# Kernel tuning notes

Hardware: AMD Instinct MI355X
Metric: run time of the kernel (lower is better)

Reference implementation:

```python
import jax, jax.numpy as jnp
import numpy as np

EMBEDDING_DIM = 256
NUM_EMBEDDINGS = 8192
COMMITMENT_COST = 0.25
DECAY = 0.99
EPSILON = 1e-5


def setup_inputs() -> dict:
    key = jax.random.key(0)
    k1, k2 = jax.random.split(key)
    inputs = jax.random.normal(k1, (16, 32, 32, EMBEDDING_DIM), dtype=jnp.float32)
    # VarianceScaling(distribution='uniform'), fan_in scaling over [D, K]
    limit = float(np.sqrt(3.0 / EMBEDDING_DIM))
    embeddings = jax.random.uniform(k2, (EMBEDDING_DIM, NUM_EMBEDDINGS),
                                    minval=-limit, maxval=limit, dtype=jnp.float32)
    return {
        'inputs': inputs,
        'embeddings': embeddings,
        'ema_cs_hidden': jnp.zeros((NUM_EMBEDDINGS,), jnp.float32),
        'ema_dw_hidden': embeddings,  # hk initializes ema_dw to the embeddings
        'counter': 0,
        'is_training': 1,
    }


def reference(inputs, embeddings, ema_cs_hidden, ema_dw_hidden, counter, is_training):
    flat = inputs.reshape(-1, EMBEDDING_DIM)                        # [N, D]
    distances = (jnp.sum(flat ** 2, axis=1, keepdims=True)
                 - 2.0 * (flat @ embeddings)
                 + jnp.sum(embeddings ** 2, axis=0, keepdims=True))  # [N, K]
    encoding_indices = jnp.argmax(-distances, axis=1)                # [N]
    encodings = jax.nn.one_hot(encoding_indices, NUM_EMBEDDINGS,
                               dtype=distances.dtype)                # [N, K]
    idx = encoding_indices.reshape(inputs.shape[:-1])
    quantized = embeddings.T[idx]                                    # gather codebook
    e_latent_loss = jnp.mean((jax.lax.stop_gradient(quantized) - inputs) ** 2)
    loss = COMMITMENT_COST * e_latent_loss

    if is_training:
        # haiku ExponentialMovingAverage with zero-debias
        new_counter = counter + 1
        debias = 1.0 - DECAY ** new_counter
        cs_hidden = ema_cs_hidden * DECAY + jnp.sum(encodings, axis=0) * (1.0 - DECAY)
        cs_avg = cs_hidden / debias                                  # [K]
        dw = flat.T @ encodings                                      # [D, K] scatter-add as GEMM
        dw_hidden = ema_dw_hidden * DECAY + dw * (1.0 - DECAY)
        dw_avg = dw_hidden / debias
        n = jnp.sum(cs_avg)
        cs_norm = (cs_avg + EPSILON) / (n + NUM_EMBEDDINGS * EPSILON) * n
        new_embeddings = dw_avg / cs_norm[None, :]                   # [D, K]
    else:
        new_embeddings = embeddings

    # straight-through estimator
    quantized_st = inputs + jax.lax.stop_gradient(quantized - inputs)
    avg_probs = jnp.mean(encodings, axis=0)
    perplexity = jnp.exp(-jnp.sum(avg_probs * jnp.log(avg_probs + 1e-10)))
    return (quantized_st, loss, perplexity, idx, new_embeddings)
```

## Files before the change

### kernel.cpp

```cpp
#include <hip/hip_runtime.h>
#include <math.h>

#define DD 256
#define KK 8192
#define NN 16384
#define DECAYF 0.99f
#define EPSF 1e-5f
#define TAU 4e-3f

#define O_Q    0
#define O_LOSS 4194304
#define O_PERP 4194305
#define O_IDX  4194306
#define O_EMB  4210690

typedef float f32x4 __attribute__((ext_vector_type(4)));
typedef _Float16 f16x8 __attribute__((ext_vector_type(8)));

__device__ __forceinline__ unsigned short f2h(float f) {
  union { _Float16 h; unsigned short u; } c;
  c.h = (_Float16)f;
  return c.u;
}

__device__ __forceinline__ void gll16(const void* g, void* l) {
  __builtin_amdgcn_global_load_lds((const __attribute__((address_space(1))) void*)g,
                                   (__attribute__((address_space(3))) void*)l, 16, 0, 0);
}

#define DPPI(x, ctrl) __builtin_amdgcn_update_dpp((x), (x), (ctrl), 0xf, 0xf, true)
#define DPPF(x, ctrl) __int_as_float(__builtin_amdgcn_update_dpp(__float_as_int(x), __float_as_int(x), (ctrl), 0xf, 0xf, true))

__global__ void k_convert_xe(const float* __restrict__ x, unsigned short* __restrict__ Ah,
                             const float* __restrict__ emb, unsigned short* __restrict__ Eh,
                             float* __restrict__ embT, float* __restrict__ esqp,
                             unsigned long long* __restrict__ keysR,
                             float* __restrict__ counts, float* __restrict__ loss_part,
                             int* __restrict__ listc) {
  __shared__ float ld[32 * 33];
  int bx = blockIdx.x;
  int t = threadIdx.x;
  if (bx < 4096) {
    int i = bx * 256 + t;
    float4 v = ((const float4*)x)[i];
    ushort4 h;
    h.x = f2h(v.x); h.y = f2h(v.y); h.z = f2h(v.z); h.w = f2h(v.w);
    ((ushort4*)Ah)[i] = h;
    if (bx < 64) {
      keysR[bx * 256 + t] = ~0ull;
    } else if (bx < 96) {
      counts[(bx - 64) * 256 + t] = 0.f;
    } else if (bx == 96) {
      loss_part[t] = 0.f;
      if (t == 0) *listc = 0;
    }
    return;
  }
  int eb = bx - 4096;
  int k0 = (eb & 255) * 32, d0b = eb >> 8;
  {
    int din = t >> 3, kq = (t & 7) * 4;
    float4 v = *(const float4*)(emb + (size_t)(d0b * 32 + din) * KK + k0 + kq);
    ld[din * 33 + kq + 0] = v.x; ld[din * 33 + kq + 1] = v.y;
    ld[din * 33 + kq + 2] = v.z; ld[din * 33 + kq + 3] = v.w;
  }
  __syncthreads();
  int kout = t >> 3, dq = (t & 7) * 4;
  float f0 = ld[(dq + 0) * 33 + kout], f1 = ld[(dq + 1) * 33 + kout];
  float f2 = ld[(dq + 2) * 33 + kout], f3 = ld[(dq + 3) * 33 + kout];
  size_t o = (size_t)(k0 + kout) * DD + d0b * 32 + dq;
  float4 fv; fv.x = f0; fv.y = f1; fv.z = f2; fv.w = f3;
  *(float4*)(embT + o) = fv;
  ushort4 hv;
  hv.x = f2h(f0); hv.y = f2h(f1); hv.z = f2h(f2); hv.w = f2h(f3);
  *(ushort4*)(Eh + o) = hv;
  float p = (f0 * f0 + f1 * f1) + (f2 * f2 + f3 * f3);
  p += __shfl_xor(p, 1, 64);
  p += __shfl_xor(p, 2, 64);
  p += __shfl_xor(p, 4, 64);
  if ((t & 7) == 0) esqp[(size_t)(k0 + kout) * 8 + d0b] = p;
}

__launch_bounds__(256, 2)
__global__ void k_dist_mfma(const unsigned short* __restrict__ Ah, const unsigned short* __restrict__ Bh,
                            const float* __restrict__ esqp,
                            float* __restrict__ part1, float* __restrict__ part2,
                            int* __restrict__ partidx) {
  __shared__ __align__(16) unsigned short sB[8192];
  __shared__ float sEq[128];

  const int tid = threadIdx.x;
  const int w = tid >> 6, lane = tid & 63;
  const int kb = blockIdx.x, nb = blockIdx.y;
  const int row0 = nb * 128, col0 = kb * 128;
  const int m = lane & 15, q = lane >> 4;

  {
    int col = tid >> 1, half = tid & 1;
    const float4* ep = (const float4*)esqp + (size_t)(col0 + col) * 2 + half;
    float4 s = *ep;
    float p = (s.x + s.y) + (s.z + s.w);
    p += __shfl_xor(p, 1, 64);
    if (half == 0) sEq[col] = p;
  }

  size_t gB[4];
  int lbB[4];
  #pragma unroll
  for (int s = 0; s < 4; ++s) {
    int g = w * 4 + s;
    int r = g * 8 + (lane >> 3);
    int c = (lane & 7) ^ (r & 7);
    gB[s] = (size_t)(col0 + r) * DD + c * 8;
    lbB[s] = g * 512;
  }

  const unsigned short* pA0 = Ah + (size_t)(row0 + w * 32 + m) * DD + q * 8;
  const unsigned short* pA1 = pA0 + 16 * DD;

  f32x4 acc[2][8];
  #pragma unroll
  for (int i = 0; i < 2; ++i)
    #pragma unroll
    for (int j = 0; j < 8; ++j) acc[i][j] = (f32x4)0.f;

  for (int it = 0; it < 4; ++it) {
    const int d0 = it * 64;
    __syncthreads();
    #pragma unroll
    for (int s = 0; s < 4; ++s) gll16(Bh + gB[s] + d0, sB + lbB[s]);
    f16x8 a[2][2];
    #pragma unroll
    for (int kk = 0; kk < 2; ++kk) {
      a[kk][0] = *(const f16x8*)(pA0 + d0 + kk * 32);
      a[kk][1] = *(const f16x8*)(pA1 + d0 + kk * 32);
    }
    __syncthreads();
    #pragma unroll
    for (int kk = 0; kk < 2; ++kk) {
      #pragma unroll
      for (int j = 0; j < 8; ++j) {
        int cn = j * 16 + m;
        int slot = (kk * 4 + q) ^ (cn & 7);
        f16x8 b = *(const f16x8*)(sB + cn * 64 + slot * 8);
        acc[0][j] = __builtin_amdgcn_mfma_f32_16x16x32_f16(a[kk][0], b, acc[0][j], 0, 0, 0);
        acc[1][j] = __builtin_amdgcn_mfma_f32_16x16x32_f16(a[kk][1], b, acc[1][j], 0, 0, 0);
      }
    }
  }

  float eq[8];
  #pragma unroll
  for (int j = 0; j < 8; ++j) eq[j] = sEq[j * 16 + m];

  #define RSTAGE(CTRL) {                                  \
    float ov = DPPF(m1, CTRL);                            \
    int   oi = DPPI(bi, CTRL);                            \
    float o2 = DPPF(m2, CTRL);                            \
    m2 = fminf(fminf(m2, o2), fmaxf(m1, ov));             \
    bool p = ov < m1;                                     \
    m1 = fminf(m1, ov);                                   \
    bi = p ? oi : bi;                                     \
  }
  #pragma unroll
  for (int i = 0; i < 2; ++i) {
    #pragma unroll
    for (int reg = 0; reg < 4; ++reg) {
      float m1 = 3.402823466e+38f, m2 = 3.402823466e+38f;
      int bi = 0;
      #pragma unroll
      for (int j = 0; j < 8; ++j) {
        float dd = fmaf(-2.0f, acc[i][j][reg], eq[j]);
        bool p = dd < m1;
        m2 = fminf(m2, fmaxf(dd, m1));
        m1 = fminf(m1, dd);
        bi = p ? (col0 + j * 16 + m) : bi;
      }
      RSTAGE(0xB1)
      RSTAGE(0x4E)
      RSTAGE(0x141)
      RSTAGE(0x140)
      if (m == 0) {
        int prow = row0 + w * 32 + i * 16 + q * 4 + reg;
        int pidx = prow * 64 + kb;
        part1[pidx] = m1; part2[pidx] = m2; partidx[pidx] = bi;
      }
    }
  }
  #undef RSTAGE
}

__global__ void k_argmin2(float* __restrict__ part1, float* __restrict__ part2,
                          const int* __restrict__ partidx, int* __restrict__ idxw,
                          int* __restrict__ listc, int* __restrict__ list) {
  int w = threadIdx.x >> 6, l = threadIdx.x & 63;
  int row = blockIdx.x * 4 + w;
  int f = blockIdx.x * 256 + threadIdx.x;
  float m1 = part1[f], m2 = part2[f];
  int bi = partidx[f];
  part1[f] = 0.f;
  part2[f] = 0.f;
  #pragma unroll
  for (int st = 1; st < 64; st <<= 1) {
    float ov = __shfl_xor(m1, st, 64);
    int   oi = __shfl_xor(bi, st, 64);
    float o2 = __shfl_xor(m2, st, 64);
    m2 = fminf(fminf(m2, o2), fmaxf(m1, ov));
    bool p = ov < m1;
    m1 = fminf(m1, ov);
    bi = p ? oi : bi;
  }
  if (l == 0) {
    idxw[row] = bi;
    if (m2 - m1 < TAU) { int pos = atomicAdd(listc, 1); list[pos] = row; }
  }
}

__global__ void k_rescore(const float* __restrict__ x, const float* __restrict__ emb,
                          const int* __restrict__ listc, const int* __restrict__ list,
                          unsigned long long* __restrict__ keysR) {
  __shared__ float se[8192];
  __shared__ double red[256];
  const int t = threadIdx.x;
  const int k0 = blockIdx.x * 32;
  int cnt = *listc;
  if ((int)blockIdx.y >= cnt) return;
  #pragma unroll
  for (int i = 0; i < 32; ++i) {
    int elem = i * 256 + t;
    int d = elem >> 5, c = elem & 31;
    se[d * 32 + c] = emb[(size_t)d * KK + k0 + c];
  }
  __syncthreads();
  const int c = t & 31, p = t >> 5;
  for (int li = blockIdx.y; li < cnt; li += gridDim.y) {
    int row = list[li];
    const float* xr = x + (size_t)row * DD;
    double acc = 0.0;
    #pragma unroll
    for (int j = 0; j < 32; ++j) {
      int d = p * 32 + j;
      double df = (double)xr[d] - (double)se[d * 32 + c];
      acc = fma(df, df, acc);
    }
    red[c * 8 + p] = acc;
    __syncthreads();
    if (t < 64) {
      unsigned long long key = ~0ull;
      if (t < 32) {
        double dist = 0.0;
        #pragma unroll
        for (int qq = 0; qq < 8; ++qq) dist += red[t * 8 + qq];
        key = ((unsigned long long)__double_as_longlong(dist) & ~0x1FFFull)
              | (unsigned long long)(k0 + t);
      }
      #pragma unroll
      for (int s = 1; s < 64; s <<= 1) {
        unsigned long long o = __shfl_xor(key, s, 64);
        if (o < key) key = o;
      }
      if (t == 0) atomicMin(&keysR[row], key);
    }
    __syncthreads();
  }
}

__global__ void k_gather(const float* __restrict__ x, const float* __restrict__ embT,
                         const int* __restrict__ idxw, const unsigned long long* __restrict__ keysR,
                         const int* __restrict__ train,
                         float* __restrict__ outq, float* __restrict__ outidx,
                         float* __restrict__ dwT, float* __restrict__ counts,
                         float* __restrict__ loss_part) {
  int w = threadIdx.x >> 6, l = threadIdx.x & 63;
  int n = blockIdx.x * 4 + w;
  unsigned long long kv = keysR[n];
  int k = (kv != ~0ull) ? (int)(kv & 0x1FFFull) : idxw[n];
  float4 xv = ((const float4*)(x + (size_t)n * DD))[l];
  float4 qv = ((const float4*)(embT + (size_t)k * DD))[l];
  int d = l * 4;

  ((float4*)(outq + (size_t)n * DD))[l] = qv;

  float e0 = qv.x - xv.x, e1 = qv.y - xv.y, e2 = qv.z - xv.z, e3 = qv.w - xv.w;
  float ls = (e0 * e0 + e1 * e1) + (e2 * e2 + e3 * e3);

  if (*train) {
    const float wdw = 1.0f - DECAYF;
    float* base = dwT + (size_t)k * DD + d;
    atomicAdd(base + 0, xv.x * wdw);
    atomicAdd(base + 1, xv.y * wdw);
    atomicAdd(base + 2, xv.z * wdw);
    atomicAdd(base + 3, xv.w * wdw);
  }

  #pragma unroll
  for (int s = 1; s < 64; s <<= 1) ls += __shfl_xor(ls, s, 64);
  if (l == 0) {
    atomicAdd(&loss_part[blockIdx.x & 255], ls);
    atomicAdd(&counts[k], 1.0f);
    outidx[n] = (float)k;
  }
}

__global__ void k_final(const float* __restrict__ dwT, const float* __restrict__ ema_dw,
                        const float* __restrict__ emb, const float* __restrict__ counts,
                        const float* __restrict__ ema_cs, const float* __restrict__ loss_part,
                        const int* __restrict__ counter, const int* __restrict__ train,
                        float* __restrict__ out4, float* __restrict__ outloss,
                        float* __restrict__ outperp) {
  __shared__ float ld[32 * 33];
  __shared__ float s_red[4], s_l[4], s_e[4];
  __shared__ float csn_s[32];
  int t = threadIdx.x;
  int k0 = blockIdx.x * 32, d0 = blockIdx.y * 32;
  int w = t >> 6, lane = t & 63;

  if (blockIdx.x == 0 && blockIdx.y == 0) {
    float lloc = loss_part[t];
    float eloc = 0.f;
    for (int i = 0; i < 32; ++i) {
      float cc = counts[t + i * 256];
      float pp = cc * (1.0f / 16384.0f);
      eloc += pp * logf(pp + 1e-10f);
    }
    #pragma unroll
    for (int s = 1; s < 64; s <<= 1) {
      lloc += __shfl_xor(lloc, s, 64);
      eloc += __shfl_xor(eloc, s, 64);
    }
    if (lane == 0) { s_l[w] = lloc; s_e[w] = eloc; }
    __syncthreads();
    if (t == 0) {
      outloss[0] = 0.25f * (((s_l[0] + s_l[1]) + (s_l[2] + s_l[3])) / 4194304.0f);
      outperp[0] = expf(-((s_e[0] + s_e[1]) + (s_e[2] + s_e[3])));
    }
  }

  if (*train) {
    float debias = 1.0f - powf(DECAYF, (float)(*counter + 1));
    float inv = 1.0f / debias;
    float nloc = 0.f;
    for (int i = 0; i < 32; ++i) {
      int k = t + i * 256;
      nloc += fmaf(counts[k], 1.0f - DECAYF, ema_cs[k] * DECAYF);
    }
    #pragma unroll
    for (int s = 1; s < 64; s <<= 1) nloc += __shfl_xor(nloc, s, 64);
    if (lane == 0) s_red[w] = nloc;
    __syncthreads();
    float nsum = ((s_red[0] + s_red[1]) + (s_red[2] + s_red[3])) * inv;
    if (t < 32) {
      int k = k0 + t;
      float a = fmaf(counts[k], 1.0f - DECAYF, ema_cs[k] * DECAYF) * inv;
      csn_s[t] = (a + EPSF) / (nsum + 8192.0f * EPSF) * nsum;
    }
    {
      int ki = t >> 3, dq = (t & 7) * 4;
      float4 v = *(const float4*)(dwT + (size_t)(k0 + ki) * DD + d0 + dq);
      ld[ki * 33 + dq + 0] = v.x; ld[ki * 33 + dq + 1] = v.y;
      ld[ki * 33 + dq + 2] = v.z; ld[ki * 33 + dq + 3] = v.w;
    }
    __syncthreads();
    int dout = t >> 3, kq = (t & 7) * 4;
    size_t o = (size_t)(d0 + dout) * KK + k0 + kq;
    float4 e = *(const float4*)(ema_dw + o);
    float4 r;
    r.x = fmaf(e.x, DECAYF, ld[(kq + 0) * 33 + dout]) * inv / csn_s[kq + 0];
    r.y = fmaf(e.y, DECAYF, ld[(kq + 1) * 33 + dout]) * inv / csn_s[kq + 1];
    r.z = fmaf(e.z, DECAYF, ld[(kq + 2) * 33 + dout]) * inv / csn_s[kq + 2];
    r.w = fmaf(e.w, DECAYF, ld[(kq + 3) * 33 + dout]) * inv / csn_s[kq + 3];
    *(float4*)(out4 + o) = r;
  } else {
    int dout = t >> 3, kq = (t & 7) * 4;
    size_t o = (size_t)(d0 + dout) * KK + k0 + kq;
    *(float4*)(out4 + o) = *(const float4*)(emb + o);
  }
}

extern "C" void kernel_launch(void* const* d_in, const int* in_sizes, int n_in,
                              void* d_out, int out_size, void* d_ws, size_t ws_size,
                              hipStream_t stream) {
  (void)in_sizes; (void)n_in; (void)out_size; (void)ws_size;
  const float* x      = (const float*)d_in[0];
  const float* emb    = (const float*)d_in[1];
  const float* ema_cs = (const float*)d_in[2];
  const float* ema_dw = (const float*)d_in[3];
  const int*   counter = (const int*)d_in[4];
  const int*   train   = (const int*)d_in[5];

  float* out = (float*)d_out;
  float* outq    = out + O_Q;
  float* outloss = out + O_LOSS;
  float* outperp = out + O_PERP;
  float* outidx  = out + O_IDX;
  float* out4    = out + O_EMB;

  char* W = (char*)d_ws;
  unsigned short* Ah   = (unsigned short*)(W);
  unsigned short* Eh   = (unsigned short*)(W + 8388608);
  float* embT          = (float*)(W + 12582912);
  float* part1         = (float*)(W + 20971520);
  float* part2         = (float*)(W + 25165824);
  int*   partidx       = (int*)(W + 29360128);
  float* dwT           = part1;
  unsigned long long* keysR = (unsigned long long*)(W + 33554432);
  float* esqp          = (float*)(W + 33685504);
  float* counts        = (float*)(W + 33947648);
  float* loss_part     = (float*)(W + 33980416);
  int*   listc         = (int*)(W + 33981440);
  int*   list          = (int*)(W + 33981444);
  int*   idxw          = (int*)(W + 34046980);

  k_convert_xe<<<6144, 256, 0, stream>>>(x, Ah, emb, Eh, embT, esqp, keysR, counts, loss_part, listc);
  k_dist_mfma<<<dim3(64, 128), 256, 0, stream>>>(Ah, Eh, esqp, part1, part2, partidx);
  k_argmin2<<<4096, 256, 0, stream>>>(part1, part2, partidx, idxw, listc, list);
  k_rescore<<<dim3(256, 8), 256, 0, stream>>>(x, emb, listc, list, keysR);
  k_gather<<<4096, 256, 0, stream>>>(x, embT, idxw, keysR, train, outq, outidx, dwT, counts, loss_part);
  k_final<<<dim3(256, 8), 256, 0, stream>>>(dwT, ema_dw, emb, counts, ema_cs, loss_part, counter, train, out4, outloss, outperp);
}
```

Measured before the change: 361.4 us.

## Transpose argmin partials to column-major and reduce per-thread over tiles

The distance kernel now stores its per-tile min/second-min/index partials as [kb][row] instead of [row][kb]. The argmin kernel becomes one thread per row that loops over 64 tiles with coalesced loads, replacing the wave-per-row shuffle reduction. The esq load into shared memory is moved after the main MFMA loop and gets an explicit barrier. The argmin launch drops to only 64 blocks, so the serial 64-step loop may run with low parallelism, and the distance kernel's partial stores become strided.

Result: no change. 354.5 us, median of 2 (-1.9%).

```diff
diff --git a/kernel.cpp b/kernel.cpp
--- a/kernel.cpp
+++ b/kernel.cpp
@@ -95,15 +95,6 @@
   const int row0 = nb * 128, col0 = kb * 128;
   const int m = lane & 15, q = lane >> 4;
 
-  {
-    int col = tid >> 1, half = tid & 1;
-    const float4* ep = (const float4*)esqp + (size_t)(col0 + col) * 2 + half;
-    float4 s = *ep;
-    float p = (s.x + s.y) + (s.z + s.w);
-    p += __shfl_xor(p, 1, 64);
-    if (half == 0) sEq[col] = p;
-  }
-
   size_t gB[4];
   int lbB[4];
   #pragma unroll
@@ -148,6 +139,16 @@
       }
     }
   }
+
+  {
+    int col = tid >> 1, half = tid & 1;
+    const float4* ep = (const float4*)esqp + (size_t)(col0 + col) * 2 + half;
+    float4 s = *ep;
+    float p = (s.x + s.y) + (s.z + s.w);
+    p += __shfl_xor(p, 1, 64);
+    if (half == 0) sEq[col] = p;
+  }
+  __syncthreads();
 
   float eq[8];
   #pragma unroll
@@ -182,7 +183,7 @@
       RSTAGE(0x140)
       if (m == 0) {
         int prow = row0 + w * 32 + i * 16 + q * 4 + reg;
-        int pidx = prow * 64 + kb;
+        int pidx = kb * NN + prow;
         part1[pidx] = m1; part2[pidx] = m2; partidx[pidx] = bi;
       }
     }
@@ -193,27 +194,22 @@
 __global__ void k_argmin2(float* __restrict__ part1, float* __restrict__ part2,
                           const int* __restrict__ partidx, int* __restrict__ idxw,
                           int* __restrict__ listc, int* __restrict__ list) {
-  int w = threadIdx.x >> 6, l = threadIdx.x & 63;
-  int row = blockIdx.x * 4 + w;
-  int f = blockIdx.x * 256 + threadIdx.x;
-  float m1 = part1[f], m2 = part2[f];
-  int bi = partidx[f];
-  part1[f] = 0.f;
-  part2[f] = 0.f;
-  #pragma unroll
-  for (int st = 1; st < 64; st <<= 1) {
-    float ov = __shfl_xor(m1, st, 64);
-    int   oi = __shfl_xor(bi, st, 64);
-    float o2 = __shfl_xor(m2, st, 64);
-    m2 = fminf(fminf(m2, o2), fmaxf(m1, ov));
-    bool p = ov < m1;
-    m1 = fminf(m1, ov);
-    bi = p ? oi : bi;
-  }
-  if (l == 0) {
-    idxw[row] = bi;
-    if (m2 - m1 < TAU) { int pos = atomicAdd(listc, 1); list[pos] = row; }
-  }
+  int row = blockIdx.x * 256 + threadIdx.x;
+  float m1 = 3.402823466e+38f, m2 = 3.402823466e+38f;
+  int bi = 0;
+  for (int kb = 0; kb < 64; ++kb) {
+    int f = kb * NN + row;
+    float a1 = part1[f], a2 = part2[f];
+    int ai = partidx[f];
+    part1[f] = 0.f;
+    part2[f] = 0.f;
+    m2 = fminf(fminf(m2, a2), fmaxf(m1, a1));
+    bool p = a1 < m1;
+    m1 = fminf(m1, a1);
+    bi = p ? ai : bi;
+  }
+  idxw[row] = bi;
+  if (m2 - m1 < TAU) { int pos = atomicAdd(listc, 1); list[pos] = row; }
 }
 
 __global__ void k_rescore(const float* __restrict__ x, const float* __restrict__ emb,
@@ -413,7 +409,7 @@
 
   k_convert_xe<<<6144, 256, 0, stream>>>(x, Ah, emb, Eh, embT, esqp, keysR, counts, loss_part, listc);
   k_dist_mfma<<<dim3(64, 128), 256, 0, stream>>>(Ah, Eh, esqp, part1, part2, partidx);
-  k_argmin2<<<4096, 256, 0, stream>>>(part1, part2, partidx, idxw, listc, list);
+  k_argmin2<<<64, 256, 0, stream>>>(part1, part2, partidx, idxw, listc, list);
   k_rescore<<<dim3(256, 8), 256, 0, stream>>>(x, emb, listc, list, keysR);
   k_gather<<<4096, 256, 0, stream>>>(x, embT, idxw, keysR, train, outq, outidx, dwT, counts, loss_part);
   k_final<<<dim3(256, 8), 256, 0, stream>>>(dwT, ema_dw, emb, counts, ema_cs, loss_part, counter, train, out4, outloss, outperp);
```
